# Performance work log

Hardware: AMD Instinct MI355X
Metric: run time of the kernel (lower is better)

## Reference

```python
import jax, jax.numpy as jnp
import numpy as np

SIGMA_INIT = 1000.0


def setup_inputs() -> dict:
    key = jax.random.key(0)
    k1, k2, k3 = jax.random.split(key, 3)
    B, M, D, S = 1024, 209, 12288, 2
    input_data = jax.random.normal(k1, (B, D), dtype=jnp.float32)
    center = jax.random.normal(k2, (M, D), dtype=jnp.float32)
    sigma = SIGMA_INIT * jnp.ones((M,), dtype=jnp.float32)
    W = 50.0 * jax.random.normal(k3, (S, M), dtype=jnp.float32)
    b = jnp.zeros((S,), dtype=jnp.float32)
    return {"input_data": input_data, "center": center, "sigma": sigma, "W": W, "b": b}


def reference(input_data, center, sigma, W, b):
    # Euclidean distance ||x_i - c_j|| via GEMM expansion (avoids [B,M,D] diff tensor)
    x2 = jnp.sum(input_data * input_data, axis=1, keepdims=True)        # [B,1]
    c2 = jnp.sum(center * center, axis=1)[None, :]                      # [1,M]
    d2 = x2 + c2 - 2.0 * (input_data @ center.T)                        # [B,M]
    dist = jnp.sqrt(jnp.maximum(d2, 0.0))
    # Note: original divides the (non-squared) norm by sigma^2, then exp(-.)
    radial = jnp.exp(-dist / (sigma * sigma)[None, :])                  # [B,M]
    return radial @ W.T + b                                             # [B,S]
```

## Files before the change

kernel.cpp:

```cpp
#include <hip/hip_runtime.h>
#include <hip/hip_bf16.h>
#include <stdint.h>

#define B_SZ 1024
#define M_SZ 209
#define MPAD 224
#define D_SZ 12288
#define KC   48
#define KCH  256
#define BK   128
#define NIT  (KCH / BK)
#define NB   16
#define BT   64
#define NCT  14
#define SROW 224
#define SLROW (KC * SROW)

#define CBF_OFF  0u
#define XXP_OFF  (MPAD * D_SZ)
#define CCP_OFF  (XXP_OFF + B_SZ * KC * 4)
#define SLAB_OFF (CCP_OFF + MPAD * 2 * 4)

typedef __attribute__((ext_vector_type(8))) short short8;
typedef __attribute__((ext_vector_type(4))) float floatx4;

__device__ __forceinline__ uint32_t pk8x4(const float4& v) {
    int d = __builtin_amdgcn_cvt_pk_fp8_f32(v.x, v.y, 0, false);
    d     = __builtin_amdgcn_cvt_pk_fp8_f32(v.z, v.w, d, true);
    return (uint32_t)d;
}

__device__ __forceinline__ float bfbits2f(unsigned short u) {
    union { uint32_t u; float f; } cv;
    cv.u = ((uint32_t)u) << 16;
    return cv.f;
}

__device__ __forceinline__ void gload_lds16(const void* g, void* l) {
    __builtin_amdgcn_global_load_lds(
        (const __attribute__((address_space(1))) void*)g,
        (__attribute__((address_space(3))) void*)l, 16, 0, 0);
}

__global__ __launch_bounds__(256) void rbf_prep(
    const float* __restrict__ c, uint8_t* __restrict__ cf8,
    float* __restrict__ ccp)
{
    __shared__ float red[4];
    const int j = blockIdx.x >> 1, h = blockIdx.x & 1;
    const int t = threadIdx.x;
    const int base = h * (D_SZ / 2);
    uint8_t* dst = cf8 + (size_t)j * D_SZ + base;
    float s = 0.f;
    if (j < M_SZ) {
        const float* src = c + (size_t)j * D_SZ + base;
        for (int i = t * 8; i < D_SZ / 2; i += 2048) {
            float4 v0 = *(const float4*)(src + i);
            float4 v1 = *(const float4*)(src + i + 4);
            s += v0.x*v0.x + v0.y*v0.y + v0.z*v0.z + v0.w*v0.w
               + v1.x*v1.x + v1.y*v1.y + v1.z*v1.z + v1.w*v1.w;
            uint2 w = { pk8x4(v0), pk8x4(v1) };
            *(uint2*)(dst + i) = w;
        }
    } else {
        uint2 zz = {0u, 0u};
        for (int i = t * 8; i < D_SZ / 2; i += 2048) *(uint2*)(dst + i) = zz;
    }
#pragma unroll
    for (int off = 32; off > 0; off >>= 1) s += __shfl_down(s, off);
    if ((t & 63) == 0) red[t >> 6] = s;
    __syncthreads();
    if (t == 0) ccp[j * 2 + h] = red[0] + red[1] + red[2] + red[3];
}

__global__ __launch_bounds__(256, 3) void rbf_main(
    const float* __restrict__ x, const uint8_t* __restrict__ cf8,
    __hip_bfloat16* __restrict__ slab, float* __restrict__ xxp)
{
    __shared__ uint8_t sc[MPAD * BK];

    const int t    = threadIdx.x;
    const int k    = blockIdx.x;
    const int b    = blockIdx.y;
    const int wave = t >> 6, lane = t & 63;
    const int quad = lane >> 4, mrow = lane & 15;
    const int qh = quad >> 1, ql = quad & 1;
    const int s2 = (mrow >> 1) & 7;

    floatx4 acc[NCT];
    const floatx4 z4 = {0.f, 0.f, 0.f, 0.f};
#pragma unroll
    for (int i = 0; i < NCT; ++i) acc[i] = z4;

    const int oE = (((lane & 7) ^ (lane >> 4)) & 7) * 16;
    const int oO = ((((lane & 7) ^ (lane >> 4)) ^ 4) & 7) * 16;
    const uint8_t* cpbE = cf8 + (size_t)(lane >> 3) * D_SZ + (size_t)k * KCH + oE;
    const uint8_t* cpbO = cf8 + (size_t)(lane >> 3) * D_SZ + (size_t)k * KCH + oO;

#pragma unroll
    for (int jj = 0; jj < 7; ++jj) {
        const int cr = wave * 7 + jj;
        const uint8_t* p = ((cr & 1) ? cpbO : cpbE) + (size_t)cr * 8 * D_SZ;
        gload_lds16(p, &sc[cr * 1024]);
    }

    const float* xr = x + (size_t)(b * BT + wave * 16 + mrow) * D_SZ
                    + (size_t)k * KCH + quad * 8;
    long xa[8];
    float sxx = 0.f;
#pragma unroll
    for (int half = 0; half < 2; ++half) {
        float4 fa[4], fb[4];
#pragma unroll
        for (int u = 0; u < 4; ++u) {
            const int ci = half * 4 + u;
            const int fo = (ci >> 2) * 128 + (ci & 3) * 32;
            fa[u] = *(const float4*)(xr + fo);
            fb[u] = *(const float4*)(xr + fo + 4);
        }
#pragma unroll
        for (int u = 0; u < 4; ++u) {
            sxx += fa[u].x*fa[u].x + fa[u].y*fa[u].y + fa[u].z*fa[u].z + fa[u].w*fa[u].w
                 + fb[u].x*fb[u].x + fb[u].y*fb[u].y + fb[u].z*fb[u].z + fb[u].w*fb[u].w;
            const uint32_t lo = pk8x4(fa[u]);
            const uint32_t hi = pk8x4(fb[u]);
            xa[half * 4 + u] = (long)(((uint64_t)hi << 32) | lo);
        }
    }

    int boff[4];
#pragma unroll
    for (int ks = 0; ks < 4; ++ks)
        boff[ks] = (((ks * 2 + qh) ^ s2) * 16) + ql * 8;
    const uint8_t* bbase = &sc[mrow * BK];

    for (int it = 0; it < NIT; ++it) {
        __syncthreads();
#pragma unroll
        for (int ks = 0; ks < 4; ++ks) {
            const long a = xa[it * 4 + ks];
#pragma unroll
            for (int ct = 0; ct < NCT; ++ct) {
                const long bv = *(const long*)(bbase + ct * 16 * BK + boff[ks]);
                acc[ct] = __builtin_amdgcn_mfma_f32_16x16x32_fp8_fp8(a, bv, acc[ct], 0, 0, 0);
            }
        }
        __syncthreads();
        if (it + 1 < NIT) {
#pragma unroll
            for (int jj = 0; jj < 7; ++jj) {
                const int cr = wave * 7 + jj;
                const uint8_t* p = ((cr & 1) ? cpbO : cpbE)
                                 + (size_t)cr * 8 * D_SZ + (it + 1) * BK;
                gload_lds16(p, &sc[cr * 1024]);
            }
        }
    }

    __hip_bfloat16* sd = slab + (size_t)k * SROW;
    const int gi0 = b * BT + wave * 16 + quad * 4;
#pragma unroll
    for (int ct = 0; ct < NCT; ++ct) {
        const int gj = ct * 16 + mrow;
#pragma unroll
        for (int rg = 0; rg < 4; ++rg)
            sd[(size_t)(gi0 + rg) * SLROW + gj] = __float2bfloat16(acc[ct][rg]);
    }

    sxx += __shfl_down(sxx, 32);
    sxx += __shfl_down(sxx, 16);
    if (lane < 16)
        xxp[(size_t)(b * BT + wave * 16 + lane) * KC + k] = sxx;
}

__global__ __launch_bounds__(256) void rbf_fin(
    const __hip_bfloat16* __restrict__ slab, const float* __restrict__ xxp,
    const float* __restrict__ ccp, const float* __restrict__ sigma,
    const float* __restrict__ W, const float* __restrict__ bias,
    float* __restrict__ out)
{
    __shared__ float jpart[MPAD * 9];
    __shared__ float jtot[MPAD];
    __shared__ float xsh;

    const int t = threadIdx.x;
    const int i = blockIdx.x;

    if (t < 64) {
        float xv = (t < KC) ? xxp[(size_t)i * KC + t] : 0.f;
#pragma unroll
        for (int off = 32; off > 0; off >>= 1) xv += __shfl_down(xv, off);
        if (t == 0) xsh = xv;
    }

    const int o = t % 28, g = t / 28;
    if (t < 252) {
        const unsigned short* sp = (const unsigned short*)slab
                                 + (size_t)i * SLROW + o * 8;
        float s8[8] = {0.f,0.f,0.f,0.f,0.f,0.f,0.f,0.f};
        for (int kk = g; kk < KC; kk += 9) {
            short8 v = *(const short8*)(sp + kk * SROW);
#pragma unroll
            for (int e = 0; e < 8; ++e) s8[e] += bfbits2f((unsigned short)v[e]);
        }
#pragma unroll
        for (int e = 0; e < 8; ++e) jpart[(o * 8 + e) * 9 + g] = s8[e];
    }
    __syncthreads();

    if (t < MPAD) {
        float d = 0.f;
#pragma unroll
        for (int g2 = 0; g2 < 9; ++g2) d += jpart[t * 9 + g2];
        jtot[t] = d;
    }
    __syncthreads();

    if (t < 64) {
        const float xxi = xsh;
        float a0 = 0.f, a1 = 0.f;
        for (int j = t; j < M_SZ; j += 64) {
            const float ccj = ccp[j * 2] + ccp[j * 2 + 1];
            float d2 = fmaxf(xxi + ccj - 2.f * jtot[j], 0.f);
            float sg = sigma[j];
            float rad = __expf(-sqrtf(d2) / (sg * sg));
            a0 += rad * W[j];
            a1 += rad * W[M_SZ + j];
        }
#pragma unroll
        for (int off = 32; off > 0; off >>= 1) {
            a0 += __shfl_down(a0, off);
            a1 += __shfl_down(a1, off);
        }
        if (t == 0) {
            out[i * 2 + 0] = a0 + bias[0];
            out[i * 2 + 1] = a1 + bias[1];
        }
    }
}

extern "C" void kernel_launch(void* const* d_in, const int* in_sizes, int n_in,
                              void* d_out, int out_size, void* d_ws, size_t ws_size,
                              hipStream_t stream)
{
    const float* x     = (const float*)d_in[0];
    const float* c     = (const float*)d_in[1];
    const float* sigma = (const float*)d_in[2];
    const float* W     = (const float*)d_in[3];
    const float* bias  = (const float*)d_in[4];
    float* out = (float*)d_out;

    char* ws = (char*)d_ws;
    uint8_t*        cf8  = (uint8_t*)(ws + CBF_OFF);
    float*          xxp  = (float*)(ws + XXP_OFF);
    float*          ccp  = (float*)(ws + CCP_OFF);
    __hip_bfloat16* slab = (__hip_bfloat16*)(ws + SLAB_OFF);

    rbf_prep<<<MPAD * 2, 256, 0, stream>>>(c, cf8, ccp);
    rbf_main<<<dim3(KC, NB), 256, 0, stream>>>(x, cf8, slab, xxp);
    rbf_fin<<<B_SZ, 256, 0, stream>>>(slab, xxp, ccp, sigma, W, bias, out);
}
```

Before: 111.7 us.

## Retile rbf_main with a smaller batch tile, larger K chunk, and x staged in LDS

The main GEMM kernel now uses 32 K-chunks of 384 instead of 48 of 256, and 32-row batch tiles instead of 64-row ones. The four waves are split 2x2 over row tiles and center-column halves, so each wave holds 7 accumulator tiles instead of 14. The x tile is converted to fp8 once per thread and staged through swizzled LDS, rather than each wave holding its own rows in registers. This lowers register pressure (occupancy hint raised to 4) and shrinks the partial-sum slab the finalize kernel must reduce. The cost is extra LDS traffic for the A operand and more blocks.

```diff
diff --git a/kernel.cpp b/kernel.cpp
--- a/kernel.cpp
+++ b/kernel.cpp
@@ -6,13 +6,13 @@
 #define M_SZ 209
 #define MPAD 224
 #define D_SZ 12288
-#define KC   48
-#define KCH  256
+#define KC   32
+#define KCH  384
 #define BK   128
 #define NIT  (KCH / BK)
-#define NB   16
-#define BT   64
-#define NCT  14
+#define NB   32
+#define BT   32
+#define NCT  7
 #define SROW 224
 #define SLROW (KC * SROW)
 
@@ -73,10 +73,11 @@
     if (t == 0) ccp[j * 2 + h] = red[0] + red[1] + red[2] + red[3];
 }
 
-__global__ __launch_bounds__(256, 3) void rbf_main(
+__global__ __launch_bounds__(256, 4) void rbf_main(
     const float* __restrict__ x, const uint8_t* __restrict__ cf8,
     __hip_bfloat16* __restrict__ slab, float* __restrict__ xxp)
 {
+    __shared__ uint8_t sx[BT * BK];
     __shared__ uint8_t sc[MPAD * BK];
 
     const int t    = threadIdx.x;
@@ -86,6 +87,8 @@
     const int quad = lane >> 4, mrow = lane & 15;
     const int qh = quad >> 1, ql = quad & 1;
     const int s2 = (mrow >> 1) & 7;
+    const int rt  = wave & 1;
+    const int cth = wave >> 1;
 
     floatx4 acc[NCT];
     const floatx4 z4 = {0.f, 0.f, 0.f, 0.f};
@@ -104,41 +107,39 @@
         gload_lds16(p, &sc[cr * 1024]);
     }
 
-    const float* xr = x + (size_t)(b * BT + wave * 16 + mrow) * D_SZ
-                    + (size_t)k * KCH + quad * 8;
-    long xa[8];
+    const int xr = t >> 3;
+    const int xc = t & 7;
+    const float* xp = x + (size_t)(b * BT + xr) * D_SZ + (size_t)k * KCH + xc * 16;
+
+    uint4 xw[NIT];
     float sxx = 0.f;
 #pragma unroll
-    for (int half = 0; half < 2; ++half) {
-        float4 fa[4], fb[4];
-#pragma unroll
-        for (int u = 0; u < 4; ++u) {
-            const int ci = half * 4 + u;
-            const int fo = (ci >> 2) * 128 + (ci & 3) * 32;
-            fa[u] = *(const float4*)(xr + fo);
-            fb[u] = *(const float4*)(xr + fo + 4);
-        }
-#pragma unroll
-        for (int u = 0; u < 4; ++u) {
-            sxx += fa[u].x*fa[u].x + fa[u].y*fa[u].y + fa[u].z*fa[u].z + fa[u].w*fa[u].w
-                 + fb[u].x*fb[u].x + fb[u].y*fb[u].y + fb[u].z*fb[u].z + fb[u].w*fb[u].w;
-            const uint32_t lo = pk8x4(fa[u]);
-            const uint32_t hi = pk8x4(fb[u]);
-            xa[half * 4 + u] = (long)(((uint64_t)hi << 32) | lo);
-        }
-    }
+    for (int it = 0; it < NIT; ++it) {
+        float4 v0 = *(const float4*)(xp + it * BK + 0);
+        float4 v1 = *(const float4*)(xp + it * BK + 4);
+        float4 v2 = *(const float4*)(xp + it * BK + 8);
+        float4 v3 = *(const float4*)(xp + it * BK + 12);
+        sxx += v0.x*v0.x + v0.y*v0.y + v0.z*v0.z + v0.w*v0.w
+             + v1.x*v1.x + v1.y*v1.y + v1.z*v1.z + v1.w*v1.w
+             + v2.x*v2.x + v2.y*v2.y + v2.z*v2.z + v2.w*v2.w
+             + v3.x*v3.x + v3.y*v3.y + v3.z*v3.z + v3.w*v3.w;
+        xw[it] = make_uint4(pk8x4(v0), pk8x4(v1), pk8x4(v2), pk8x4(v3));
+    }
+    uint8_t* sxw = &sx[xr * BK + ((xc ^ ((xr >> 1) & 7)) & 7) * 16];
 
     int boff[4];
 #pragma unroll
     for (int ks = 0; ks < 4; ++ks)
-        boff[ks] = (((ks * 2 + qh) ^ s2) * 16) + ql * 8;
-    const uint8_t* bbase = &sc[mrow * BK];
+        boff[ks] = (((ks * 2 + qh) ^ s2) & 7) * 16 + ql * 8;
+    const uint8_t* abase = &sx[(rt * 16 + mrow) * BK];
+    const uint8_t* bbase = &sc[(cth * 7 * 16 + mrow) * BK];
 
     for (int it = 0; it < NIT; ++it) {
+        *(uint4*)sxw = xw[it];
         __syncthreads();
 #pragma unroll
         for (int ks = 0; ks < 4; ++ks) {
-            const long a = xa[it * 4 + ks];
+            const long a = *(const long*)(abase + boff[ks]);
 #pragma unroll
             for (int ct = 0; ct < NCT; ++ct) {
                 const long bv = *(const long*)(bbase + ct * 16 * BK + boff[ks]);
@@ -158,19 +159,19 @@
     }
 
     __hip_bfloat16* sd = slab + (size_t)k * SROW;
-    const int gi0 = b * BT + wave * 16 + quad * 4;
+    const int gi0 = b * BT + rt * 16 + quad * 4;
 #pragma unroll
     for (int ct = 0; ct < NCT; ++ct) {
-        const int gj = ct * 16 + mrow;
+        const int gj = (cth * 7 + ct) * 16 + mrow;
 #pragma unroll
         for (int rg = 0; rg < 4; ++rg)
             sd[(size_t)(gi0 + rg) * SLROW + gj] = __float2bfloat16(acc[ct][rg]);
     }
 
-    sxx += __shfl_down(sxx, 32);
-    sxx += __shfl_down(sxx, 16);
-    if (lane < 16)
-        xxp[(size_t)(b * BT + wave * 16 + lane) * KC + k] = sxx;
+    sxx += __shfl_down(sxx, 4);
+    sxx += __shfl_down(sxx, 2);
+    sxx += __shfl_down(sxx, 1);
+    if ((t & 7) == 0) xxp[(size_t)(b * BT + xr) * KC + k] = sxx;
 }
 
 __global__ __launch_bounds__(256) void rbf_fin(
```

Result: no change. 110.0 us (-1.6%).
